# Kernel optimization log

Measured on AMD Instinct MI355X. Metric: run time of the kernel, lower is better.

Reference implementation:

```python
import jax, jax.numpy as jnp
import numpy as np

N_NODES = 100000
N_EDGES = 600000
N_GRAPHS = 64
D_IN = 128
D_H = 128


def setup_inputs() -> dict:
    key = jax.random.key(0)
    ks = jax.random.split(key, 12)
    x = jax.random.normal(ks[0], (N_NODES, D_IN), dtype=jnp.float32)
    edge_index = jax.random.randint(ks[1], (2, N_EDGES), 0, N_NODES, dtype=jnp.int64)
    batch = jnp.sort(jax.random.randint(ks[2], (N_NODES,), 0, N_GRAPHS, dtype=jnp.int64))
    s = 1.0 / np.sqrt(D_H)
    W1 = jax.random.normal(ks[3], (D_H, D_IN), dtype=jnp.float32) * s
    W2 = jax.random.normal(ks[4], (D_H, D_H), dtype=jnp.float32) * s
    W3 = jax.random.normal(ks[5], (D_H, D_H), dtype=jnp.float32) * s
    W4 = jax.random.normal(ks[6], (D_H, D_H), dtype=jnp.float32) * s
    Wc = jax.random.normal(ks[7], (1, D_H), dtype=jnp.float32) * s
    b1 = jnp.zeros((D_H,), jnp.float32)
    b2 = jnp.zeros((D_H,), jnp.float32)
    b3 = jnp.zeros((D_H,), jnp.float32)
    b4 = jnp.zeros((D_H,), jnp.float32)
    bc = jnp.zeros((1,), jnp.float32)
    return {"x": x, "edge_index": edge_index, "batch": batch,
            "W1": W1, "b1": b1, "W2": W2, "b2": b2,
            "W3": W3, "b3": b3, "W4": W4, "b4": b4,
            "Wc": Wc, "bc": bc}


def _conv(x, W, b, row, col, n_nodes):
    # Linear transform then sum-aggregate source features at target nodes.
    # (PyG message() returns x_j unscaled -> the degree norm in the original
    # forward is computed but never applied.)
    h = x @ W.T + b                                   # [N, D]
    return jax.ops.segment_sum(h[row], col, num_segments=n_nodes)


def reference(x, edge_index, batch, W1, b1, W2, b2, W3, b3, W4, b4, Wc, bc):
    n = x.shape[0]
    loops = jnp.arange(n, dtype=edge_index.dtype)
    row = jnp.concatenate([edge_index[0], loops])     # sources (with self loops)
    col = jnp.concatenate([edge_index[1], loops])     # targets

    h = jax.nn.relu(_conv(x, W1, b1, row, col, n))    # dropout = identity (eval)
    h = jax.nn.relu(_conv(h, W2, b2, row, col, n))
    h = jax.nn.relu(_conv(h, W3, b3, row, col, n))
    h = _conv(h, W4, b4, row, col, n)

    # global mean pool over graphs
    sums = jax.ops.segment_sum(h, batch, num_segments=N_GRAPHS)        # [G, D]
    cnts = jax.ops.segment_sum(jnp.ones((n,), h.dtype), batch, num_segments=N_GRAPHS)
    pooled = sums / jnp.maximum(cnts, 1.0)[:, None]

    return jax.nn.sigmoid(pooled @ Wc.T + bc)         # [G, 1]
```

## Files before the change

### kernel.cpp

```cpp
#include <hip/hip_runtime.h>
#include <hip/hip_bf16.h>

#define N_NODES 100000
#define N_EDGES 600000
#define N_GRAPHS 64
#define D 128

#define NBLK_SCAN ((N_NODES + 255) / 256)

typedef __attribute__((ext_vector_type(8))) short short8v;
typedef __attribute__((ext_vector_type(4))) float float4v;

__device__ __forceinline__ unsigned short f2bf(float f) {
    unsigned int u = __float_as_uint(f);
    return (unsigned short)((u + 0x7FFF + ((u >> 16) & 1)) >> 16);
}
__device__ __forceinline__ float bf2f(unsigned short h) {
    return __uint_as_float(((unsigned int)h) << 16);
}


__global__ void count_deg_k(const int* __restrict__ col, int* __restrict__ cnt) {
    int e = blockIdx.x * blockDim.x + threadIdx.x;
    if (e < N_EDGES) atomicAdd(&cnt[col[e]], 1);
}

__global__ __launch_bounds__(256) void partial_k(const int* __restrict__ cnt,
                                                 int* __restrict__ psum) {
    int i = blockIdx.x * 256 + threadIdx.x;
    int v = (i < N_NODES) ? cnt[i] : 0;
#pragma unroll
    for (int d = 32; d > 0; d >>= 1) v += __shfl_down(v, d, 64);
    __shared__ int ws[4];
    if ((threadIdx.x & 63) == 0) ws[threadIdx.x >> 6] = v;
    __syncthreads();
    if (threadIdx.x == 0) psum[blockIdx.x] = ws[0] + ws[1] + ws[2] + ws[3];
}

__global__ __launch_bounds__(512) void scanpart_k(int* __restrict__ psum) {
    __shared__ int ls[512];
    int t = threadIdx.x;
    int v = (t < NBLK_SCAN) ? psum[t] : 0;
    ls[t] = v;
    __syncthreads();
    for (int d = 1; d < 512; d <<= 1) {
        int u = (t >= d) ? ls[t - d] : 0;
        __syncthreads();
        ls[t] += u;
        __syncthreads();
    }
    if (t < NBLK_SCAN) psum[t] = ls[t] - v;
}

__global__ __launch_bounds__(256) void scan_scatter_k(const int* __restrict__ cnt,
                                                      const int* __restrict__ psum,
                                                      int* __restrict__ start) {
    int b = blockIdx.x, t = threadIdx.x;
    int i = b * 256 + t;
    int v = (i < N_NODES) ? cnt[i] : 0;
    __shared__ int ls[256];
    ls[t] = v;
    __syncthreads();
    for (int d = 1; d < 256; d <<= 1) {
        int u = (t >= d) ? ls[t - d] : 0;
        __syncthreads();
        ls[t] += u;
        __syncthreads();
    }
    int incl = ls[t];
    int off = psum[b];
    if (i < N_NODES) start[i] = off + incl - v;
    if (i == N_NODES - 1) start[N_NODES] = off + incl;
}

__global__ void fill_csr_k(const int* __restrict__ row, const int* __restrict__ col,
                           const int* __restrict__ start, int* __restrict__ fill,
                           int* __restrict__ esrc) {
    int e = blockIdx.x * blockDim.x + threadIdx.x;
    if (e < N_EDGES) {
        int c = col[e];
        int p = atomicAdd(&fill[c], 1);
        esrc[start[c] + p] = row[e];
    }
}


__global__ __launch_bounds__(128) void bounds_k(const int* __restrict__ batch,
                                                int* __restrict__ gstart) {
    int g = threadIdx.x;
    if (g > N_GRAPHS) return;
    int lo = 0, hi = N_NODES;
    while (lo < hi) {
        int mid = (lo + hi) >> 1;
        if (batch[mid] < g) lo = mid + 1; else hi = mid;
    }
    gstart[g] = lo;
}


__global__ __launch_bounds__(256) void split_k(const float* __restrict__ in,
                                               unsigned short* __restrict__ hi,
                                               unsigned short* __restrict__ lo, int n4) {
    int i = blockIdx.x * 256 + threadIdx.x;
    if (i >= n4) return;
    float4 v = reinterpret_cast<const float4*>(in)[i];
    ushort4 h, l;
    h.x = f2bf(v.x); l.x = f2bf(v.x - bf2f(h.x));
    h.y = f2bf(v.y); l.y = f2bf(v.y - bf2f(h.y));
    h.z = f2bf(v.z); l.z = f2bf(v.z - bf2f(h.z));
    h.w = f2bf(v.w); l.w = f2bf(v.w - bf2f(h.w));
    reinterpret_cast<ushort4*>(hi)[i] = h;
    reinterpret_cast<ushort4*>(lo)[i] = l;
}


#define BM 128

__global__ __launch_bounds__(256) void gemm_mfma_k(
    const unsigned short* __restrict__ Ahi, const unsigned short* __restrict__ Alo,
    const unsigned short* __restrict__ Whi, const unsigned short* __restrict__ Wlo,
    const float* __restrict__ bias, float* __restrict__ out, int nrows) {
    __shared__ float swp[4][32][132];
    const int tid = threadIdx.x, l = tid & 63, wv = tid >> 6;
    const int bm0 = blockIdx.x * BM;
    const int g = l >> 4, li = l & 15;

    float4v acc[2][8];
#pragma unroll
    for (int rg = 0; rg < 2; ++rg)
#pragma unroll
        for (int cg = 0; cg < 8; ++cg) acc[rg][cg] = (float4v){0.f, 0.f, 0.f, 0.f};

    size_t abase[2];
#pragma unroll
    for (int rg = 0; rg < 2; ++rg)
        abase[rg] = (size_t)min(bm0 + wv * 32 + rg * 16 + li, nrows - 1) * D + g * 8;

#pragma unroll
    for (int kk = 0; kk < 4; ++kk) {
        const int k0 = kk * 32;
        short8v ah[2], al[2];
#pragma unroll
        for (int rg = 0; rg < 2; ++rg) {
            ah[rg] = *reinterpret_cast<const short8v*>(Ahi + abase[rg] + k0);
            al[rg] = *reinterpret_cast<const short8v*>(Alo + abase[rg] + k0);
        }
#pragma unroll
        for (int cg = 0; cg < 8; ++cg) {
            const size_t wb = (size_t)(cg * 16 + li) * D + g * 8 + k0;
            short8v wh = *reinterpret_cast<const short8v*>(Whi + wb);
            short8v wl = *reinterpret_cast<const short8v*>(Wlo + wb);
#pragma unroll
            for (int rg = 0; rg < 2; ++rg) {
                acc[rg][cg] = __builtin_amdgcn_mfma_f32_16x16x32_bf16(ah[rg], wh, acc[rg][cg], 0, 0, 0);
                acc[rg][cg] = __builtin_amdgcn_mfma_f32_16x16x32_bf16(al[rg], wh, acc[rg][cg], 0, 0, 0);
                acc[rg][cg] = __builtin_amdgcn_mfma_f32_16x16x32_bf16(ah[rg], wl, acc[rg][cg], 0, 0, 0);
                acc[rg][cg] = __builtin_amdgcn_mfma_f32_16x16x32_bf16(al[rg], wl, acc[rg][cg], 0, 0, 0);
            }
        }
    }

#pragma unroll
    for (int rg = 0; rg < 2; ++rg)
#pragma unroll
        for (int cg = 0; cg < 8; ++cg)
#pragma unroll
            for (int r = 0; r < 4; ++r)
                swp[wv][rg * 16 + g * 4 + r][cg * 16 + li] = acc[rg][cg][r];

    const int c4 = l & 31, rh = l >> 5;
    const float4 bias_v = *reinterpret_cast<const float4*>(&bias[c4 * 4]);
#pragma unroll
    for (int it = 0; it < 16; ++it) {
        int rowl = it * 2 + rh;
        int grow = bm0 + wv * 32 + rowl;
        if (grow < nrows) {
            float4 v = *reinterpret_cast<const float4*>(&swp[wv][rowl][c4 * 4]);
            v.x += bias_v.x; v.y += bias_v.y; v.z += bias_v.z; v.w += bias_v.w;
            *reinterpret_cast<float4*>(&out[(size_t)grow * D + c4 * 4]) = v;
        }
    }
}


__global__ __launch_bounds__(256) void aggregate_k(const float* __restrict__ t,
                                                   const int* __restrict__ start,
                                                   const int* __restrict__ esrc,
                                                   unsigned short* __restrict__ ohi,
                                                   unsigned short* __restrict__ olo,
                                                   int do_relu) {
    const int wv = threadIdx.x >> 6, l = threadIdx.x & 63;
    const int node = blockIdx.x * 4 + wv;
    if (node >= N_NODES) return;
    const int s = start[node], e = start[node + 1];
    const size_t base = ((size_t)node << 7) + 2 * l;
    float2 acc = *reinterpret_cast<const float2*>(t + base);
    int i = s;
    for (; i + 1 < e; i += 2) {
        const float2 v0 = *reinterpret_cast<const float2*>(t + (((size_t)esrc[i] << 7) + 2 * l));
        const float2 v1 = *reinterpret_cast<const float2*>(t + (((size_t)esrc[i + 1] << 7) + 2 * l));
        acc.x += v0.x + v1.x;
        acc.y += v0.y + v1.y;
    }
    if (i < e) {
        const float2 v = *reinterpret_cast<const float2*>(t + (((size_t)esrc[i] << 7) + 2 * l));
        acc.x += v.x;
        acc.y += v.y;
    }
    if (do_relu) {
        acc.x = fmaxf(acc.x, 0.f);
        acc.y = fmaxf(acc.y, 0.f);
    }
    unsigned short hx = f2bf(acc.x), hy = f2bf(acc.y);
    unsigned short lx = f2bf(acc.x - bf2f(hx)), ly = f2bf(acc.y - bf2f(hy));
    *reinterpret_cast<unsigned int*>(ohi + base) = (unsigned int)hx | ((unsigned int)hy << 16);
    *reinterpret_cast<unsigned int*>(olo + base) = (unsigned int)lx | ((unsigned int)ly << 16);
}


__global__ __launch_bounds__(128) void vbeta_k(const float* __restrict__ W4,
                                               const float* __restrict__ b4,
                                               const float* __restrict__ Wc,
                                               float* __restrict__ vbeta) {
    int k = threadIdx.x;
    float acc = 0.f;
    for (int j = 0; j < D; ++j) acc = fmaf(Wc[j], W4[j * D + k], acc);
    vbeta[k] = acc;
    __shared__ float red[128];
    red[k] = Wc[k] * b4[k];
    __syncthreads();
    for (int st = 64; st > 0; st >>= 1) {
        if (k < st) red[k] += red[k + st];
        __syncthreads();
    }
    if (k == 0) vbeta[D] = red[0];
}

__global__ __launch_bounds__(256) void matvec_k(const unsigned short* __restrict__ hhi,
                                                const unsigned short* __restrict__ hlo,
                                                const float* __restrict__ vbeta,
                                                float* __restrict__ s) {
    int wid = threadIdx.x >> 6, lane = threadIdx.x & 63;
    int row = blockIdx.x * 4 + wid;
    const size_t base = (size_t)row * D + lane * 2;
    unsigned int h2 = *reinterpret_cast<const unsigned int*>(hhi + base);
    unsigned int l2 = *reinterpret_cast<const unsigned int*>(hlo + base);
    float hx = bf2f((unsigned short)h2) + bf2f((unsigned short)l2);
    float hy = bf2f((unsigned short)(h2 >> 16)) + bf2f((unsigned short)(l2 >> 16));
    const float2 vv = *reinterpret_cast<const float2*>(&vbeta[lane * 2]);
    float dot = fmaf(hx, vv.x, hy * vv.y);
#pragma unroll
    for (int d = 32; d > 0; d >>= 1) dot += __shfl_down(dot, d, 64);
    if (lane == 0) s[row] = dot;
}

__global__ __launch_bounds__(256) void sagg_k(const float* __restrict__ s,
                                              const int* __restrict__ start,
                                              const int* __restrict__ esrc,
                                              const float* __restrict__ vbeta,
                                              float* __restrict__ a) {
    int i = blockIdx.x * 256 + threadIdx.x;
    if (i >= N_NODES) return;
    int s0 = start[i], s1 = start[i + 1];
    float beta = vbeta[D];
    float acc = s[i] + (float)(1 + s1 - s0) * beta;
    for (int e = s0; e < s1; ++e) acc += s[esrc[e]];
    a[i] = acc;
}

__global__ __launch_bounds__(256) void spool_k(const float* __restrict__ a,
                                               const int* __restrict__ gstart,
                                               const float* __restrict__ bc,
                                               float* __restrict__ out) {
    int g = blockIdx.x;
    int lo = gstart[g], hi = gstart[g + 1];
    float acc = 0.f;
    for (int i = lo + threadIdx.x; i < hi; i += 256) acc += a[i];
    __shared__ float red[256];
    red[threadIdx.x] = acc;
    __syncthreads();
    for (int st = 128; st > 0; st >>= 1) {
        if (threadIdx.x < st) red[threadIdx.x] += red[threadIdx.x + st];
        __syncthreads();
    }
    if (threadIdx.x == 0) {
        float c = (float)max(hi - lo, 1);
        out[g] = 1.f / (1.f + expf(-(red[0] / c + bc[0])));
    }
}


extern "C" void kernel_launch(void* const* d_in, const int* in_sizes, int n_in,
                              void* d_out, int out_size, void* d_ws, size_t ws_size,
                              hipStream_t stream) {
    const float* x   = (const float*)d_in[0];
    const int* ei    = (const int*)d_in[1];
    const int* batch = (const int*)d_in[2];
    const float* W1  = (const float*)d_in[3];
    const float* b1  = (const float*)d_in[4];
    const float* W2  = (const float*)d_in[5];
    const float* b2  = (const float*)d_in[6];
    const float* W3  = (const float*)d_in[7];
    const float* b3  = (const float*)d_in[8];
    const float* W4  = (const float*)d_in[9];
    const float* b4  = (const float*)d_in[10];
    const float* Wc  = (const float*)d_in[11];
    const float* bc  = (const float*)d_in[12];
    float* out = (float*)d_out;

    const int* row = ei;
    const int* col = ei + N_EDGES;

    char* p = (char*)d_ws;
    float* t = (float*)p;            p += (size_t)N_NODES * D * 4;
    unsigned short* hhi = (unsigned short*)p; p += (size_t)N_NODES * D * 2;
    unsigned short* hlo = (unsigned short*)p; p += (size_t)N_NODES * D * 2;
    unsigned short* whi = (unsigned short*)p; p += (size_t)D * D * 2;
    unsigned short* wlo = (unsigned short*)p; p += (size_t)D * D * 2;
    int* esrc = (int*)p;             p += (size_t)N_EDGES * 4;
    int* cstart = (int*)p;           p += ((N_NODES + 1) * 4 + 15) / 16 * 16;
    int* cfill = (int*)p;            p += (size_t)N_NODES * 4;
    int* psum = (int*)p;             p += ((NBLK_SCAN + 3) / 4) * 16;
    int* gstart = (int*)p;           p += 256;

    float* vbeta = t;
    float* s_arr = t + 256;
    float* a_arr = t + 256 + N_NODES;

    hipMemsetAsync(cfill, 0, (size_t)N_NODES * 4, stream);
    count_deg_k<<<(N_EDGES + 255) / 256, 256, 0, stream>>>(col, cfill);
    partial_k<<<NBLK_SCAN, 256, 0, stream>>>(cfill, psum);
    scanpart_k<<<1, 512, 0, stream>>>(psum);
    scan_scatter_k<<<NBLK_SCAN, 256, 0, stream>>>(cfill, psum, cstart);
    hipMemsetAsync(cfill, 0, (size_t)N_NODES * 4, stream);
    fill_csr_k<<<(N_EDGES + 255) / 256, 256, 0, stream>>>(row, col, cstart, cfill, esrc);

    bounds_k<<<1, 128, 0, stream>>>(batch, gstart);

    const int ggrid = (N_NODES + BM - 1) / BM;
    const int agrid = (N_NODES + 3) / 4;
    const int xn4 = N_NODES * D / 4;
    const int wn4 = D * D / 4;

    split_k<<<(xn4 + 255) / 256, 256, 0, stream>>>(x, hhi, hlo, xn4);
    split_k<<<(wn4 + 255) / 256, 256, 0, stream>>>(W1, whi, wlo, wn4);
    gemm_mfma_k<<<ggrid, 256, 0, stream>>>(hhi, hlo, whi, wlo, b1, t, N_NODES);
    aggregate_k<<<agrid, 256, 0, stream>>>(t, cstart, esrc, hhi, hlo, 1);
    split_k<<<(wn4 + 255) / 256, 256, 0, stream>>>(W2, whi, wlo, wn4);
    gemm_mfma_k<<<ggrid, 256, 0, stream>>>(hhi, hlo, whi, wlo, b2, t, N_NODES);
    aggregate_k<<<agrid, 256, 0, stream>>>(t, cstart, esrc, hhi, hlo, 1);
    split_k<<<(wn4 + 255) / 256, 256, 0, stream>>>(W3, whi, wlo, wn4);
    gemm_mfma_k<<<ggrid, 256, 0, stream>>>(hhi, hlo, whi, wlo, b3, t, N_NODES);
    aggregate_k<<<agrid, 256, 0, stream>>>(t, cstart, esrc, hhi, hlo, 1);

    vbeta_k<<<1, 128, 0, stream>>>(W4, b4, Wc, vbeta);
    matvec_k<<<N_NODES / 4, 256, 0, stream>>>(hhi, hlo, vbeta, s_arr);
    sagg_k<<<(N_NODES + 255) / 256, 256, 0, stream>>>(s_arr, cstart, esrc, vbeta, a_arr);
    spool_k<<<N_GRAPHS, 256, 0, stream>>>(a_arr, gstart, bc, out);
}
```

Measured before the change: 443.2 us.

## Fuse aggregation before GEMM per layer using linearity of sum-aggregate

Reorders each conv layer to aggregate input features over neighbours first (A·X then W), using linearity and scaling the bias by 1+degree, and fuses aggregation, bf16 hi/lo split, MFMA GEMM, bias and ReLU into one kernel. This removes the fp32 intermediate write/read of the transformed features, the separate split kernel for x, and the hi/lo activation buffers, keeping activations in fp32 ping-pong buffers. The gather now runs on fp32 inputs inside the GEMM kernel, which may limit occupancy because of the large shared tile and mixes latency-bound gathers with the MFMA work.

```diff
diff --git a/kernel.cpp b/kernel.cpp
--- a/kernel.cpp
+++ b/kernel.cpp
@@ -114,107 +114,108 @@
 }
 
 
-#define BM 128
-
-__global__ __launch_bounds__(256) void gemm_mfma_k(
-    const unsigned short* __restrict__ Ahi, const unsigned short* __restrict__ Alo,
+#define FTILE 64
+#define FPITCH 132
+
+__global__ __launch_bounds__(256) void fused_layer_k(
+    const float* __restrict__ hin,
     const unsigned short* __restrict__ Whi, const unsigned short* __restrict__ Wlo,
-    const float* __restrict__ bias, float* __restrict__ out, int nrows) {
-    __shared__ float swp[4][32][132];
-    const int tid = threadIdx.x, l = tid & 63, wv = tid >> 6;
-    const int bm0 = blockIdx.x * BM;
-    const int g = l >> 4, li = l & 15;
-
-    float4v acc[2][8];
-#pragma unroll
-    for (int rg = 0; rg < 2; ++rg)
-#pragma unroll
-        for (int cg = 0; cg < 8; ++cg) acc[rg][cg] = (float4v){0.f, 0.f, 0.f, 0.f};
-
-    size_t abase[2];
-#pragma unroll
-    for (int rg = 0; rg < 2; ++rg)
-        abase[rg] = (size_t)min(bm0 + wv * 32 + rg * 16 + li, nrows - 1) * D + g * 8;
+    const float* __restrict__ bias,
+    const int* __restrict__ start, const int* __restrict__ esrc,
+    float* __restrict__ hout) {
+    __shared__ float tile[FTILE * FPITCH];
+    __shared__ float scnt[FTILE];
+    const int tid = threadIdx.x;
+    const int n0 = blockIdx.x * FTILE;
+
+    {
+        const int hw = tid >> 5, li = tid & 31;
+        for (int it = 0; it < 8; ++it) {
+            const int r = it * 8 + hw;
+            const int node = n0 + r;
+            float4 acc = make_float4(0.f, 0.f, 0.f, 0.f);
+            int deg = 0;
+            if (node < N_NODES) {
+                const int s = start[node], e = start[node + 1];
+                deg = e - s;
+                acc = *reinterpret_cast<const float4*>(hin + ((size_t)node << 7) + 4 * li);
+                int i = s;
+                for (; i + 3 < e; i += 4) {
+                    const float4 v0 = *reinterpret_cast<const float4*>(hin + (((size_t)esrc[i] << 7) + 4 * li));
+                    const float4 v1 = *reinterpret_cast<const float4*>(hin + (((size_t)esrc[i + 1] << 7) + 4 * li));
+                    const float4 v2 = *reinterpret_cast<const float4*>(hin + (((size_t)esrc[i + 2] << 7) + 4 * li));
+                    const float4 v3 = *reinterpret_cast<const float4*>(hin + (((size_t)esrc[i + 3] << 7) + 4 * li));
+                    acc.x += (v0.x + v1.x) + (v2.x + v3.x);
+                    acc.y += (v0.y + v1.y) + (v2.y + v3.y);
+                    acc.z += (v0.z + v1.z) + (v2.z + v3.z);
+                    acc.w += (v0.w + v1.w) + (v2.w + v3.w);
+                }
+                for (; i < e; ++i) {
+                    const float4 v = *reinterpret_cast<const float4*>(hin + (((size_t)esrc[i] << 7) + 4 * li));
+                    acc.x += v.x; acc.y += v.y; acc.z += v.z; acc.w += v.w;
+                }
+            }
+            *reinterpret_cast<float4*>(&tile[r * FPITCH + 4 * li]) = acc;
+            if (li == 0) scnt[r] = (float)(1 + deg);
+        }
+    }
+    __syncthreads();
+
+    const int l = tid & 63, wv = tid >> 6;
+    const int g = l >> 4, li16 = l & 15;
+
+    float4v acc[8];
+#pragma unroll
+    for (int cg = 0; cg < 8; ++cg) acc[cg] = (float4v){0.f, 0.f, 0.f, 0.f};
 
 #pragma unroll
     for (int kk = 0; kk < 4; ++kk) {
         const int k0 = kk * 32;
-        short8v ah[2], al[2];
-#pragma unroll
-        for (int rg = 0; rg < 2; ++rg) {
-            ah[rg] = *reinterpret_cast<const short8v*>(Ahi + abase[rg] + k0);
-            al[rg] = *reinterpret_cast<const short8v*>(Alo + abase[rg] + k0);
+        const float* tp = &tile[(wv * 16 + li16) * FPITCH + k0 + g * 8];
+        float4 f0 = *reinterpret_cast<const float4*>(tp);
+        float4 f1 = *reinterpret_cast<const float4*>(tp + 4);
+        float fv[8] = {f0.x, f0.y, f0.z, f0.w, f1.x, f1.y, f1.z, f1.w};
+        short8v ah, al;
+#pragma unroll
+        for (int j = 0; j < 8; ++j) {
+            unsigned short h = f2bf(fv[j]);
+            ah[j] = (short)h;
+            al[j] = (short)f2bf(fv[j] - bf2f(h));
         }
 #pragma unroll
         for (int cg = 0; cg < 8; ++cg) {
-            const size_t wb = (size_t)(cg * 16 + li) * D + g * 8 + k0;
+            const size_t wb = (size_t)(cg * 16 + li16) * D + g * 8 + k0;
             short8v wh = *reinterpret_cast<const short8v*>(Whi + wb);
             short8v wl = *reinterpret_cast<const short8v*>(Wlo + wb);
-#pragma unroll
-            for (int rg = 0; rg < 2; ++rg) {
-                acc[rg][cg] = __builtin_amdgcn_mfma_f32_16x16x32_bf16(ah[rg], wh, acc[rg][cg], 0, 0, 0);
-                acc[rg][cg] = __builtin_amdgcn_mfma_f32_16x16x32_bf16(al[rg], wh, acc[rg][cg], 0, 0, 0);
-                acc[rg][cg] = __builtin_amdgcn_mfma_f32_16x16x32_bf16(ah[rg], wl, acc[rg][cg], 0, 0, 0);
-                acc[rg][cg] = __builtin_amdgcn_mfma_f32_16x16x32_bf16(al[rg], wl, acc[rg][cg], 0, 0, 0);
-            }
+            acc[cg] = __builtin_amdgcn_mfma_f32_16x16x32_bf16(ah, wh, acc[cg], 0, 0, 0);
+            acc[cg] = __builtin_amdgcn_mfma_f32_16x16x32_bf16(al, wh, acc[cg], 0, 0, 0);
+            acc[cg] = __builtin_amdgcn_mfma_f32_16x16x32_bf16(ah, wl, acc[cg], 0, 0, 0);
+            acc[cg] = __builtin_amdgcn_mfma_f32_16x16x32_bf16(al, wl, acc[cg], 0, 0, 0);
         }
     }
 
 #pragma unroll
-    for (int rg = 0; rg < 2; ++rg)
-#pragma unroll
-        for (int cg = 0; cg < 8; ++cg)
-#pragma unroll
-            for (int r = 0; r < 4; ++r)
-                swp[wv][rg * 16 + g * 4 + r][cg * 16 + li] = acc[rg][cg][r];
+    for (int cg = 0; cg < 8; ++cg)
+#pragma unroll
+        for (int r = 0; r < 4; ++r)
+            tile[(wv * 16 + g * 4 + r) * FPITCH + cg * 16 + li16] = acc[cg][r];
 
     const int c4 = l & 31, rh = l >> 5;
-    const float4 bias_v = *reinterpret_cast<const float4*>(&bias[c4 * 4]);
-#pragma unroll
-    for (int it = 0; it < 16; ++it) {
-        int rowl = it * 2 + rh;
-        int grow = bm0 + wv * 32 + rowl;
-        if (grow < nrows) {
-            float4 v = *reinterpret_cast<const float4*>(&swp[wv][rowl][c4 * 4]);
-            v.x += bias_v.x; v.y += bias_v.y; v.z += bias_v.z; v.w += bias_v.w;
-            *reinterpret_cast<float4*>(&out[(size_t)grow * D + c4 * 4]) = v;
+    const float4 bv = *reinterpret_cast<const float4*>(&bias[4 * c4]);
+#pragma unroll
+    for (int it = 0; it < 8; ++it) {
+        const int rowl = wv * 16 + it * 2 + rh;
+        const int grow = n0 + rowl;
+        if (grow < N_NODES) {
+            float4 v = *reinterpret_cast<const float4*>(&tile[rowl * FPITCH + 4 * c4]);
+            const float c = scnt[rowl];
+            v.x = fmaxf(fmaf(c, bv.x, v.x), 0.f);
+            v.y = fmaxf(fmaf(c, bv.y, v.y), 0.f);
+            v.z = fmaxf(fmaf(c, bv.z, v.z), 0.f);
+            v.w = fmaxf(fmaf(c, bv.w, v.w), 0.f);
+            *reinterpret_cast<float4*>(&hout[(size_t)grow * D + 4 * c4]) = v;
         }
     }
-}
-
-
-__global__ __launch_bounds__(256) void aggregate_k(const float* __restrict__ t,
-                                                   const int* __restrict__ start,
-                                                   const int* __restrict__ esrc,
-                                                   unsigned short* __restrict__ ohi,
-                                                   unsigned short* __restrict__ olo,
-                                                   int do_relu) {
-    const int wv = threadIdx.x >> 6, l = threadIdx.x & 63;
-    const int node = blockIdx.x * 4 + wv;
-    if (node >= N_NODES) return;
-    const int s = start[node], e = start[node + 1];
-    const size_t base = ((size_t)node << 7) + 2 * l;
-    float2 acc = *reinterpret_cast<const float2*>(t + base);
-    int i = s;
-    for (; i + 1 < e; i += 2) {
-        const float2 v0 = *reinterpret_cast<const float2*>(t + (((size_t)esrc[i] << 7) + 2 * l));
-        const float2 v1 = *reinterpret_cast<const float2*>(t + (((size_t)esrc[i + 1] << 7) + 2 * l));
-        acc.x += v0.x + v1.x;
-        acc.y += v0.y + v1.y;
-    }
-    if (i < e) {
-        const float2 v = *reinterpret_cast<const float2*>(t + (((size_t)esrc[i] << 7) + 2 * l));
-        acc.x += v.x;
-        acc.y += v.y;
-    }
-    if (do_relu) {
-        acc.x = fmaxf(acc.x, 0.f);
-        acc.y = fmaxf(acc.y, 0.f);
-    }
-    unsigned short hx = f2bf(acc.x), hy = f2bf(acc.y);
-    unsigned short lx = f2bf(acc.x - bf2f(hx)), ly = f2bf(acc.y - bf2f(hy));
-    *reinterpret_cast<unsigned int*>(ohi + base) = (unsigned int)hx | ((unsigned int)hy << 16);
-    *reinterpret_cast<unsigned int*>(olo + base) = (unsigned int)lx | ((unsigned int)ly << 16);
 }
 
 
@@ -236,19 +237,14 @@
     if (k == 0) vbeta[D] = red[0];
 }
 
-__global__ __launch_bounds__(256) void matvec_k(const unsigned short* __restrict__ hhi,
-                                                const unsigned short* __restrict__ hlo,
+__global__ __launch_bounds__(256) void matvec_k(const float* __restrict__ h,
                                                 const float* __restrict__ vbeta,
                                                 float* __restrict__ s) {
     int wid = threadIdx.x >> 6, lane = threadIdx.x & 63;
     int row = blockIdx.x * 4 + wid;
-    const size_t base = (size_t)row * D + lane * 2;
-    unsigned int h2 = *reinterpret_cast<const unsigned int*>(hhi + base);
-    unsigned int l2 = *reinterpret_cast<const unsigned int*>(hlo + base);
-    float hx = bf2f((unsigned short)h2) + bf2f((unsigned short)l2);
-    float hy = bf2f((unsigned short)(h2 >> 16)) + bf2f((unsigned short)(l2 >> 16));
+    const float2 hv = *reinterpret_cast<const float2*>(&h[(size_t)row * D + lane * 2]);
     const float2 vv = *reinterpret_cast<const float2*>(&vbeta[lane * 2]);
-    float dot = fmaf(hx, vv.x, hy * vv.y);
+    float dot = fmaf(hv.x, vv.x, hv.y * vv.y);
 #pragma unroll
     for (int d = 32; d > 0; d >>= 1) dot += __shfl_down(dot, d, 64);
     if (lane == 0) s[row] = dot;
@@ -312,9 +308,8 @@
     const int* col = ei + N_EDGES;
 
     char* p = (char*)d_ws;
-    float* t = (float*)p;            p += (size_t)N_NODES * D * 4;
-    unsigned short* hhi = (unsigned short*)p; p += (size_t)N_NODES * D * 2;
-    unsigned short* hlo = (unsigned short*)p; p += (size_t)N_NODES * D * 2;
+    float* hA = (float*)p;           p += (size_t)N_NODES * D * 4;
+    float* hB = (float*)p;           p += (size_t)N_NODES * D * 4;
     unsigned short* whi = (unsigned short*)p; p += (size_t)D * D * 2;
     unsigned short* wlo = (unsigned short*)p; p += (size_t)D * D * 2;
     int* esrc = (int*)p;             p += (size_t)N_EDGES * 4;
@@ -323,9 +318,9 @@
     int* psum = (int*)p;             p += ((NBLK_SCAN + 3) / 4) * 16;
     int* gstart = (int*)p;           p += 256;
 
-    float* vbeta = t;
-    float* s_arr = t + 256;
-    float* a_arr = t + 256 + N_NODES;
+    float* vbeta = hB;
+    float* s_arr = hB + 256;
+    float* a_arr = hB + 256 + N_NODES;
 
     hipMemsetAsync(cfill, 0, (size_t)N_NODES * 4, stream);
     count_deg_k<<<(N_EDGES + 255) / 256, 256, 0, stream>>>(col, cfill);
@@ -337,24 +332,18 @@
 
     bounds_k<<<1, 128, 0, stream>>>(batch, gstart);
 
-    const int ggrid = (N_NODES + BM - 1) / BM;
-    const int agrid = (N_NODES + 3) / 4;
-    const int xn4 = N_NODES * D / 4;
+    const int fgrid = (N_NODES + FTILE - 1) / FTILE;
     const int wn4 = D * D / 4;
 
-    split_k<<<(xn4 + 255) / 256, 256, 0, stream>>>(x, hhi, hlo, xn4);
     split_k<<<(wn4 + 255) / 256, 256, 0, stream>>>(W1, whi, wlo, wn4);
-    gemm_mfma_k<<<ggrid, 256, 0, stream>>>(hhi, hlo, whi, wlo, b1, t, N_NODES);
-    aggregate_k<<<agrid, 256, 0, stream>>>(t, cstart, esrc, hhi, hlo, 1);
+    fused_layer_k<<<fgrid, 256, 0, stream>>>(x, whi, wlo, b1, cstart, esrc, hA);
     split_k<<<(wn4 + 255) / 256, 256, 0, stream>>>(W2, whi, wlo, wn4);
-    gemm_mfma_k<<<ggrid, 256, 0, stream>>>(hhi, hlo, whi, wlo, b2, t, N_NODES);
-    aggregate_k<<<agrid, 256, 0, stream>>>(t, cstart, esrc, hhi, hlo, 1);
+    fused_layer_k<<<fgrid, 256, 0, stream>>>(hA, whi, wlo, b2, cstart, esrc, hB);
     split_k<<<(wn4 + 255) / 256, 256, 0, stream>>>(W3, whi, wlo, wn4);
-    gemm_mfma_k<<<ggrid, 256, 0, stream>>>(hhi, hlo, whi, wlo, b3, t, N_NODES);
-    aggregate_k<<<agrid, 256, 0, stream>>>(t, cstart, esrc, hhi, hlo, 1);
+    fused_layer_k<<<fgrid, 256, 0, stream>>>(hB, whi, wlo, b3, cstart, esrc, hA);
 
     vbeta_k<<<1, 128, 0, stream>>>(W4, b4, Wc, vbeta);
-    matvec_k<<<N_NODES / 4, 256, 0, stream>>>(hhi, hlo, vbeta, s_arr);
+    matvec_k<<<N_NODES / 4, 256, 0, stream>>>(hA, vbeta, s_arr);
     sagg_k<<<(N_NODES + 255) / 256, 256, 0, stream>>>(s_arr, cstart, esrc, vbeta, a_arr);
     spool_k<<<N_GRAPHS, 256, 0, stream>>>(a_arr, gstart, bc, out);
 }
```

After: 482.3 us. 1.09x slower.
